# Kernel tuning notes

Hardware: AMD Instinct MI355X
Metric: run time of the kernel (lower is better)

## Reference

```python
import jax, jax.numpy as jnp
import numpy as np

INF = 1.0e6
SIGMA = 1.0
RADIUS = 2.5
M, N, H, K, C_IN, C_OUT = 50000, 50000, 32, 15, 128, 128
EXTENT = 10.0  # spatial extent of the random point cloud


def setup_inputs() -> dict:
    key = jax.random.key(0)
    k1, k2, k3, k4, k5, k6 = jax.random.split(key, 6)
    q_pts = jax.random.uniform(k1, (M, 3), dtype=jnp.float32) * EXTENT
    s_pts = jax.random.uniform(k2, (N, 3), dtype=jnp.float32) * EXTENT
    s_feats = jax.random.normal(k3, (N, C_IN), dtype=jnp.float32)
    neighb_inds = jax.random.randint(k4, (M, H), 0, N, dtype=jnp.int64)
    # kernel points: random points inside sphere of given radius (stand-in for load_kernels)
    kp = jax.random.normal(k5, (K, 3), dtype=jnp.float32)
    kp = kp / jnp.linalg.norm(kp, axis=1, keepdims=True) * (RADIUS * 0.66)
    kernel_points = kp.at[0].set(0.0)  # fixed center point
    # kaiming-uniform-like init
    bound = 1.0 / np.sqrt(C_IN)
    weights = jax.random.uniform(k6, (K, C_IN, C_OUT), dtype=jnp.float32,
                                 minval=-bound, maxval=bound)
    return {"q_pts": q_pts, "s_pts": s_pts, "s_feats": s_feats,
            "neighb_inds": neighb_inds, "kernel_points": kernel_points,
            "weights": weights}


def reference(q_pts, s_pts, s_feats, neighb_inds, kernel_points, weights):
    # pad support points with a far-away point so out-of-range indices get zero influence
    s_pts_pad = jnp.concatenate([s_pts, jnp.full((1, 3), INF, s_pts.dtype)], axis=0)
    neighbors = s_pts_pad[neighb_inds] - q_pts[:, None, :]          # (M, H, 3)
    diffs = neighbors[:, :, None, :] - kernel_points[None, None]    # (M, H, K, 3)
    sq_dist = jnp.sum(diffs * diffs, axis=-1)                       # (M, H, K)
    # linear influence, clipped at 0 (no_grad in torch -> stop_gradient here)
    w = jnp.clip(1.0 - jnp.sqrt(sq_dist) / SIGMA, 0.0)              # (M, H, K)
    neighbor_weights = jax.lax.stop_gradient(jnp.swapaxes(w, 1, 2)) # (M, K, H)
    # gather neighbor features (padded with a zero row)
    feats_pad = jnp.concatenate([s_feats, jnp.zeros((1, s_feats.shape[1]), s_feats.dtype)], axis=0)
    neighbor_feats = feats_pad[neighb_inds]                         # (M, H, C_in)
    weighted_feats = jnp.matmul(neighbor_weights, neighbor_feats)   # (M, K, C_in)
    return jnp.einsum('mkc,kcd->md', weighted_feats, weights)       # (M, C_out)
```

## Files before the change

kernel.cpp:

```cpp
#include <hip/hip_runtime.h>

#define M_Q 50000
#define N_S 50000
#define H_N 32
#define K_P 15
#define C_IN 128
#define C_OUT 128

#define G_QB 64
#define G_NT 256
#define NB_GEO ((M_Q + G_QB - 1) / G_QB)
#define LCAP 64

#define WTF_SLOTS (K_P * 8 * 4 * 64)
#define NB_WCVT (WTF_SLOTS / 256)

#define ENT 96
#define SUBT (ENT / 16)
#define CAPK 12288
#define K2_TILES (CAPK / ENT)

#define WS_WTF_OFF 256
#define WS_WTF_BYTES (WTF_SLOTS * 16)
#define WS_BKT_OFF (WS_WTF_OFF + WS_WTF_BYTES)
#define WS_BKT_BYTES (K_P * CAPK * 8)
#define WS_NEED (WS_BKT_OFF + WS_BKT_BYTES)

typedef __attribute__((ext_vector_type(8))) short s8v;
typedef __attribute__((ext_vector_type(4))) float f4v;
typedef __attribute__((ext_vector_type(4))) float fl4;
typedef __attribute__((ext_vector_type(4))) unsigned u4v;

static __device__ __forceinline__ unsigned f2bf_bits(float x) {
    union { float f; unsigned u; } v; v.f = x;
    return (v.u + 0x7fffu + ((v.u >> 16) & 1u)) >> 16;
}
static __device__ __forceinline__ unsigned pack_bf16(float a, float b) {
    return f2bf_bits(a) | (f2bf_bits(b) << 16);
}

template <typename IT>
__global__ __launch_bounds__(G_NT, 4) void k1_geom(
    const float* __restrict__ q_pts,
    const float* __restrict__ s_pts,
    const IT* __restrict__ inds,
    const float* __restrict__ kp,
    const float* __restrict__ W,
    unsigned* __restrict__ ws_u)
{
    const int b = blockIdx.x;
    const int t = threadIdx.x;

    if (b >= NB_GEO) {
        const int i = (b - NB_GEO) * 256 + t;
        if (i < WTF_SLOTS) {
            const int lane = i & 63;
            const int kk = (i >> 6) & 3;
            const int col = (i >> 8) & 7;
            const int k = i >> 11;
            const int d = col * 16 + (lane & 15);
            const int c0 = kk * 32 + (lane >> 4) * 8;
            unsigned short* dst =
                (unsigned short*)((char*)ws_u + WS_WTF_OFF) + (size_t)i * 8;
            #pragma unroll
            for (int j = 0; j < 8; ++j)
                dst[j] = (unsigned short)f2bf_bits(W[((size_t)k * 128 + c0 + j) * 128 + d]);
        }
        return;
    }

    __shared__ int s_lcnt[K_P];
    __shared__ uint2 s_le[K_P][LCAP];
    __shared__ int s_gb[K_P], s_gc[K_P];

    float kpx[K_P], kpy[K_P], kpz[K_P];
    #pragma unroll
    for (int k = 0; k < K_P; ++k) {
        kpx[k] = kp[k * 3 + 0];
        kpy[k] = kp[k * 3 + 1];
        kpz[k] = kp[k * 3 + 2];
    }

    if (t < K_P) s_lcnt[t] = 0;
    __syncthreads();

    const int qbase = b * G_QB;
    const int lane = t & 63;

    int idxv[8], qgv[8];
    #pragma unroll
    for (int it = 0; it < 8; ++it) {
        const int task = it * G_NT + t;
        const int q = task >> 5, h = task & 31;
        const int qg = qbase + q;
        qgv[it] = qg;
        long long idx = (qg < M_Q) ? (long long)inds[(size_t)qg * H_N + h]
                                   : (long long)N_S;
        idxv[it] = ((unsigned long long)idx < (unsigned long long)N_S) ? (int)idx : -1;
    }
    float px[8], py[8], pz[8], qx[8], qy[8], qz[8];
    #pragma unroll
    for (int it = 0; it < 8; ++it) {
        const int i32 = (idxv[it] >= 0) ? idxv[it] : 0;
        px[it] = s_pts[i32 * 3 + 0];
        py[it] = s_pts[i32 * 3 + 1];
        pz[it] = s_pts[i32 * 3 + 2];
        const int qg = (qgv[it] < M_Q) ? qgv[it] : (M_Q - 1);
        qx[it] = q_pts[qg * 3 + 0];
        qy[it] = q_pts[qg * 3 + 1];
        qz[it] = q_pts[qg * 3 + 2];
    }

    #pragma unroll
    for (int it = 0; it < 8; ++it) {
        const bool valid = (idxv[it] >= 0) & (qgv[it] < M_Q);
        const float rx = valid ? px[it] - qx[it] : 1.0e6f;
        const float ry = valid ? py[it] - qy[it] : 1.0e6f;
        const float rz = valid ? pz[it] - qz[it] : 1.0e6f;
        #pragma unroll
        for (int k = 0; k < K_P; ++k) {
            const float dx = rx - kpx[k];
            const float dy = ry - kpy[k];
            const float dz = rz - kpz[k];
            const float d2 = dx * dx + dy * dy + dz * dz;
            const bool hit = d2 < 1.0f;
            const unsigned long long mask = __ballot(hit);
            if (mask) {
                const int leader = __builtin_ctzll(mask);
                int base = 0;
                if (lane == leader)
                    base = atomicAdd(&s_lcnt[k], (int)__builtin_popcountll(mask));
                base = __shfl(base, leader);
                if (hit) {
                    const int pos = base +
                        (int)__builtin_popcountll(mask & ((1ull << lane) - 1ull));
                    if (pos < LCAP)
                        s_le[k][pos] = make_uint2(
                            ((unsigned)qgv[it] << 16) | (unsigned)idxv[it],
                            __float_as_uint(1.0f - sqrtf(d2)));
                }
            }
        }
    }
    __syncthreads();

    if (t < K_P) {
        const int cl = min(s_lcnt[t], LCAP);
        const int base = (int)atomicAdd(&ws_u[t], (unsigned)cl);
        s_gb[t] = base;
        const int avail = CAPK - base;
        s_gc[t] = max(0, min(cl, avail));
    }
    __syncthreads();

    uint2* bkt = (uint2*)((char*)ws_u + WS_BKT_OFF);
    #pragma unroll
    for (int k = 0; k < K_P; ++k) {
        if (t < s_gc[k])
            bkt[(size_t)k * CAPK + s_gb[k] + t] = s_le[k][t];
    }
}

__global__ __launch_bounds__(256, 3) void k2_gemm(
    const float* __restrict__ s_feats,
    const unsigned* __restrict__ ws_u,
    float* __restrict__ out)
{
    const int k = blockIdx.x;
    const int base = blockIdx.y * ENT;
    const int cnt = min((int)ws_u[k], CAPK);
    int n_e = cnt - base;
    if (n_e <= 0) return;
    if (n_e > ENT) n_e = ENT;

    __shared__ unsigned short s_A[SUBT * 4 * 64 * 8];
    __shared__ unsigned s_mi[ENT];

    const int t = threadIdx.x;
    const int lane = t & 63;
    const int w = t >> 6;
    const int quad = lane >> 4, l15 = lane & 15;

    const unsigned short* Wtf = (const unsigned short*)((const char*)ws_u + WS_WTF_OFF);
    s8v bf[2][4];
    #pragma unroll
    for (int nc = 0; nc < 2; ++nc)
        #pragma unroll
        for (int kk = 0; kk < 4; ++kk)
            bf[nc][kk] = *(const s8v*)(Wtf +
                ((((size_t)k * 8 + (w * 2 + nc)) * 4 + kk) * 64 + lane) * 8);

    const int e = t >> 1, half = t & 1;
    if (e < ENT) {
        const int sub = e >> 4, l15e = e & 15;
        if (e < n_e) {
            const uint2* bkt = (const uint2*)((const char*)ws_u + WS_BKT_OFF)
                               + (size_t)k * CAPK + base;
            const uint2 be = bkt[e];
            const unsigned mi = be.x;
            const float wgt = __uint_as_float(be.y);
            if (half == 0) s_mi[e] = mi;
            const float* fr = s_feats + (size_t)(mi & 0xffffu) * C_IN + half * 64;
            #pragma unroll
            for (int j = 0; j < 4; ++j) {
                const fl4 fa = *(const fl4*)(fr + j * 16);
                const fl4 fb = *(const fl4*)(fr + j * 16 + 4);
                const fl4 fc = *(const fl4*)(fr + j * 16 + 8);
                const fl4 fd = *(const fl4*)(fr + j * 16 + 12);
                u4v g0, g1;
                g0[0] = pack_bf16(wgt * fa.x, wgt * fa.y);
                g0[1] = pack_bf16(wgt * fa.z, wgt * fa.w);
                g0[2] = pack_bf16(wgt * fb.x, wgt * fb.y);
                g0[3] = pack_bf16(wgt * fb.z, wgt * fb.w);
                g1[0] = pack_bf16(wgt * fc.x, wgt * fc.y);
                g1[1] = pack_bf16(wgt * fc.z, wgt * fc.w);
                g1[2] = pack_bf16(wgt * fd.x, wgt * fd.y);
                g1[3] = pack_bf16(wgt * fd.z, wgt * fd.w);
                const int cs = half * 64 + j * 16;
                const int kk = cs >> 5;
                const int qd = (cs >> 3) & 3;
                *(u4v*)&s_A[(size_t)(((sub * 4 + kk) * 64) + qd * 16 + l15e) * 8] = g0;
                *(u4v*)&s_A[(size_t)(((sub * 4 + kk) * 64) + (qd + 1) * 16 + l15e) * 8] = g1;
            }
        } else {
            if (half == 0) s_mi[e] = 0xffffffffu;
            const u4v z = {0u, 0u, 0u, 0u};
            #pragma unroll
            for (int j = 0; j < 4; ++j) {
                const int cs = half * 64 + j * 16;
                const int kk = cs >> 5;
                const int qd = (cs >> 3) & 3;
                *(u4v*)&s_A[(size_t)(((sub * 4 + kk) * 64) + qd * 16 + l15e) * 8] = z;
                *(u4v*)&s_A[(size_t)(((sub * 4 + kk) * 64) + (qd + 1) * 16 + l15e) * 8] = z;
            }
        }
    }
    __syncthreads();

    const f4v zf = {0.0f, 0.0f, 0.0f, 0.0f};
    f4v acc[SUBT][2];
    #pragma unroll
    for (int s = 0; s < SUBT; ++s) { acc[s][0] = zf; acc[s][1] = zf; }

    #pragma unroll
    for (int s = 0; s < SUBT; ++s) {
        s8v af[4];
        #pragma unroll
        for (int kk = 0; kk < 4; ++kk)
            af[kk] = *(const s8v*)&s_A[(size_t)((s * 4 + kk) * 64 + lane) * 8];
        #pragma unroll
        for (int nc = 0; nc < 2; ++nc)
            #pragma unroll
            for (int kk = 0; kk < 4; ++kk)
                acc[s][nc] = __builtin_amdgcn_mfma_f32_16x16x32_bf16(
                    af[kk], bf[nc][kk], acc[s][nc], 0, 0, 0);
    }

    #pragma unroll
    for (int s = 0; s < SUBT; ++s) {
        #pragma unroll
        for (int r = 0; r < 4; ++r) {
            const unsigned mi = s_mi[s * 16 + quad * 4 + r];
            const unsigned m = mi >> 16;
            if (m < M_Q) {
                float* op = out + (size_t)m * C_OUT + w * 32 + l15;
                atomicAdd(op,      acc[s][0][r]);
                atomicAdd(op + 16, acc[s][1][r]);
            }
        }
    }
}

template <typename IT>
__global__ __launch_bounds__(128, 8) void kpconv_v1(
    const float* __restrict__ q_pts, const float* __restrict__ s_pts,
    const float* __restrict__ s_feats, const IT* __restrict__ neighb_inds,
    const float* __restrict__ kernel_points, const float* __restrict__ weights,
    float* __restrict__ out)
{
    __shared__ float s_kp[K_P * 3];
    __shared__ float s_w[K_P][H_N];
    __shared__ int s_idx[H_N];
    __shared__ unsigned s_hmask, s_kmask;
    __shared__ float s_wf[K_P][C_IN];
    const int m = blockIdx.x, tid = threadIdx.x;
    if (tid < K_P * 3) s_kp[tid] = kernel_points[tid];
    if (tid == 0) { s_hmask = 0u; s_kmask = 0u; }
    __syncthreads();
    if (tid < H_N) {
        long long idx = (long long)neighb_inds[(size_t)m * H_N + tid];
        const float qx = q_pts[m * 3], qy = q_pts[m * 3 + 1], qz = q_pts[m * 3 + 2];
        float rx, ry, rz; int idx32;
        if ((unsigned long long)idx < (unsigned long long)N_S) {
            idx32 = (int)idx;
            rx = s_pts[idx32 * 3] - qx; ry = s_pts[idx32 * 3 + 1] - qy; rz = s_pts[idx32 * 3 + 2] - qz;
        } else { idx32 = 0; rx = ry = rz = 1.0e6f; }
        s_idx[tid] = idx32;
        unsigned kmask = 0u;
        #pragma unroll
        for (int k = 0; k < K_P; ++k) {
            const float dx = rx - s_kp[k * 3], dy = ry - s_kp[k * 3 + 1], dz = rz - s_kp[k * 3 + 2];
            const float w = fmaxf(1.0f - sqrtf(dx * dx + dy * dy + dz * dz), 0.0f);
            s_w[k][tid] = w;
            if (w > 0.0f) kmask |= (1u << k);
        }
        if (kmask) { atomicOr(&s_hmask, 1u << tid); atomicOr(&s_kmask, kmask); }
    }
    __syncthreads();
    const unsigned hmask = s_hmask, kmask = s_kmask;
    float wf[K_P];
    #pragma unroll
    for (int k = 0; k < K_P; ++k) wf[k] = 0.0f;
    unsigned hmv = hmask;
    while (hmv) {
        const int h = __builtin_ctz(hmv); hmv &= hmv - 1;
        const float f = s_feats[(size_t)s_idx[h] * C_IN + tid];
        #pragma unroll
        for (int k = 0; k < K_P; ++k) wf[k] = fmaf(s_w[k][h], f, wf[k]);
    }
    #pragma unroll
    for (int k = 0; k < K_P; ++k) s_wf[k][tid] = wf[k];
    __syncthreads();
    float a = 0.0f;
    unsigned km = kmask;
    while (km) {
        const int k = __builtin_ctz(km); km &= km - 1;
        const float* Wk = weights + (size_t)k * C_IN * C_OUT + tid;
        #pragma unroll 8
        for (int c = 0; c < C_IN; ++c) a = fmaf(s_wf[k][c], Wk[(size_t)c * C_OUT], a);
    }
    out[(size_t)m * C_OUT + tid] = a;
}

extern "C" void kernel_launch(void* const* d_in, const int* in_sizes, int n_in,
                              void* d_out, int out_size, void* d_ws, size_t ws_size,
                              hipStream_t stream) {
    const float* q_pts         = (const float*)d_in[0];
    const float* s_pts         = (const float*)d_in[1];
    const float* s_feats       = (const float*)d_in[2];
    const float* kernel_points = (const float*)d_in[4];
    const float* weights       = (const float*)d_in[5];
    float* out = (float*)d_out;
    const bool i64 = (in_sizes[3] == 2 * M_Q * H_N);

    if (ws_size < (size_t)WS_NEED) {
        dim3 grid(M_Q), block(128);
        if (i64)
            kpconv_v1<long long><<<grid, block, 0, stream>>>(
                q_pts, s_pts, s_feats, (const long long*)d_in[3], kernel_points, weights, out);
        else
            kpconv_v1<int><<<grid, block, 0, stream>>>(
                q_pts, s_pts, s_feats, (const int*)d_in[3], kernel_points, weights, out);
        return;
    }

    unsigned* ws_u = (unsigned*)d_ws;
    hipMemsetAsync(d_ws, 0, 64, stream);
    hipMemsetAsync(d_out, 0, (size_t)out_size * sizeof(float), stream);

    dim3 g1(NB_GEO + NB_WCVT), b1(G_NT);
    if (i64)
        k1_geom<long long><<<g1, b1, 0, stream>>>(
            q_pts, s_pts, (const long long*)d_in[3], kernel_points, weights, ws_u);
    else
        k1_geom<int><<<g1, b1, 0, stream>>>(
            q_pts, s_pts, (const int*)d_in[3], kernel_points, weights, ws_u);

    dim3 g2(K_P, K2_TILES), b2(256);
    k2_gemm<<<g2, b2, 0, stream>>>(s_feats, ws_u, out);
}
```

Baseline: 160.5 us.

## Replace scattered float atomics with scratch writes plus per-query gather reduction

The GEMM kernel stops doing atomicAdd scatter into the output for bucketed entries. Instead it writes each entry's 128-wide partial result to a scratch buffer, while the geometry kernel records, for each query, a list of scratch positions. A new reduce kernel sums those rows per query, and an overflow kernel handles lists that exceed capacity. The aim is to remove global float-atomic contention and traffic, at the cost of a large scratch workspace, extra memsets and two more kernel launches.

```diff
diff --git a/kernel.cpp b/kernel.cpp
--- a/kernel.cpp
+++ b/kernel.cpp
@@ -19,12 +19,18 @@
 #define SUBT (ENT / 16)
 #define CAPK 12288
 #define K2_TILES (CAPK / ENT)
-
-#define WS_WTF_OFF 256
-#define WS_WTF_BYTES (WTF_SLOTS * 16)
-#define WS_BKT_OFF (WS_WTF_OFF + WS_WTF_BYTES)
-#define WS_BKT_BYTES (K_P * CAPK * 8)
-#define WS_NEED (WS_BKT_OFF + WS_BKT_BYTES)
+#define SCAP 8192
+#define MLCAP 16
+#define OVFCAP 4096
+
+#define WS_WTF_OFF 128
+#define WS_BKT_OFF 491648
+#define WS_MLC_OFF 1966336
+#define WS_ML_OFF  2166784
+#define WS_OVF_OFF 5366784
+#define WS_SCR_OFF 5399552
+#define WS_NEED_SMALL 1966208
+#define WS_NEED_FULL  68314112ULL
 
 typedef __attribute__((ext_vector_type(8))) short s8v;
 typedef __attribute__((ext_vector_type(4))) float f4v;
@@ -46,7 +52,8 @@
     const IT* __restrict__ inds,
     const float* __restrict__ kp,
     const float* __restrict__ W,
-    unsigned* __restrict__ ws_u)
+    unsigned* __restrict__ ws_u,
+    const int do_full)
 {
     const int b = blockIdx.x;
     const int t = threadIdx.x;
@@ -154,17 +161,34 @@
     __syncthreads();
 
     uint2* bkt = (uint2*)((char*)ws_u + WS_BKT_OFF);
+    unsigned* ml_cnt = ws_u + (WS_MLC_OFF >> 2);
+    unsigned* ml = ws_u + (WS_ML_OFF >> 2);
+    uint2* ovf = (uint2*)((char*)ws_u + WS_OVF_OFF);
     #pragma unroll
     for (int k = 0; k < K_P; ++k) {
-        if (t < s_gc[k])
-            bkt[(size_t)k * CAPK + s_gb[k] + t] = s_le[k][t];
+        if (t < s_gc[k]) {
+            const uint2 ent = s_le[k][t];
+            const int pos = s_gb[k] + t;
+            bkt[(size_t)k * CAPK + pos] = ent;
+            if (do_full && pos < SCAP) {
+                const unsigned m = ent.x >> 16;
+                const unsigned gpos = (unsigned)(k * SCAP + pos);
+                const unsigned j = atomicAdd(&ml_cnt[m], 1u);
+                if (j < MLCAP) ml[(size_t)m * MLCAP + j] = gpos;
+                else {
+                    const unsigned o = atomicAdd(&ws_u[15], 1u);
+                    if (o < OVFCAP) ovf[o] = make_uint2(m, gpos);
+                }
+            }
+        }
     }
 }
 
 __global__ __launch_bounds__(256, 3) void k2_gemm(
     const float* __restrict__ s_feats,
-    const unsigned* __restrict__ ws_u,
-    float* __restrict__ out)
+    unsigned* __restrict__ ws_u,
+    float* __restrict__ out,
+    const int do_full)
 {
     const int k = blockIdx.x;
     const int base = blockIdx.y * ENT;
@@ -180,6 +204,8 @@
     const int lane = t & 63;
     const int w = t >> 6;
     const int quad = lane >> 4, l15 = lane & 15;
+
+    if (do_full && t == 0 && base + n_e > SCAP) atomicAdd(&ws_u[16], 1u);
 
     const unsigned short* Wtf = (const unsigned short*)((const char*)ws_u + WS_WTF_OFF);
     s8v bf[2][4];
@@ -256,19 +282,77 @@
                     af[kk], bf[nc][kk], acc[s][nc], 0, 0, 0);
     }
 
+    float* scratch = (float*)((char*)ws_u + WS_SCR_OFF);
     #pragma unroll
     for (int s = 0; s < SUBT; ++s) {
         #pragma unroll
         for (int r = 0; r < 4; ++r) {
-            const unsigned mi = s_mi[s * 16 + quad * 4 + r];
-            const unsigned m = mi >> 16;
-            if (m < M_Q) {
-                float* op = out + (size_t)m * C_OUT + w * 32 + l15;
-                atomicAdd(op,      acc[s][0][r]);
-                atomicAdd(op + 16, acc[s][1][r]);
+            const int er = s * 16 + quad * 4 + r;
+            if (er < n_e) {
+                const int pos = base + er;
+                if (do_full && pos < SCAP) {
+                    float* sp = scratch + ((size_t)k * SCAP + pos) * 128 + w * 32 + l15;
+                    sp[0]  = acc[s][0][r];
+                    sp[16] = acc[s][1][r];
+                } else {
+                    const unsigned m = s_mi[er] >> 16;
+                    float* op = out + (size_t)m * C_OUT + w * 32 + l15;
+                    atomicAdd(op,      acc[s][0][r]);
+                    atomicAdd(op + 16, acc[s][1][r]);
+                }
             }
         }
     }
+}
+
+__global__ __launch_bounds__(128) void k4_ovf(
+    const unsigned* __restrict__ ws_u, float* __restrict__ out)
+{
+    const float* scratch = (const float*)((const char*)ws_u + WS_SCR_OFF);
+    const uint2* ovf = (const uint2*)((const char*)ws_u + WS_OVF_OFF);
+    unsigned n = ws_u[15];
+    if (n > OVFCAP) n = OVFCAP;
+    for (unsigned i = blockIdx.x; i < n; i += gridDim.x) {
+        const uint2 e = ovf[i];
+        atomicAdd(out + (size_t)e.x * C_OUT + threadIdx.x,
+                  scratch[(size_t)e.y * 128 + threadIdx.x]);
+    }
+}
+
+__global__ __launch_bounds__(256, 4) void k3_reduce(
+    const unsigned* __restrict__ ws_u, float* __restrict__ out)
+{
+    const float* scratch = (const float*)((const char*)ws_u + WS_SCR_OFF);
+    const unsigned* ml_cnt = ws_u + (WS_MLC_OFF >> 2);
+    const unsigned* ml = ws_u + (WS_ML_OFF >> 2);
+
+    const int t = threadIdx.x;
+    const int m = blockIdx.x * 64 + (t >> 2);
+    const int sub = t & 3;
+    if (m >= M_Q) return;
+
+    const bool rd = (ws_u[15] != 0u) || (ws_u[16] != 0u);
+    int cnt = (int)ml_cnt[m];
+    if (cnt > MLCAP) cnt = MLCAP;
+
+    float* op = out + (size_t)m * C_OUT + sub * 32;
+    fl4 a[8];
+    if (rd) {
+        #pragma unroll
+        for (int i = 0; i < 8; ++i) a[i] = ((const fl4*)op)[i];
+    } else {
+        const fl4 z = {0.0f, 0.0f, 0.0f, 0.0f};
+        #pragma unroll
+        for (int i = 0; i < 8; ++i) a[i] = z;
+    }
+    for (int j = 0; j < cnt; ++j) {
+        const unsigned gpos = ml[(size_t)m * MLCAP + j];
+        const fl4* sp = (const fl4*)(scratch + (size_t)gpos * 128 + sub * 32);
+        #pragma unroll
+        for (int i = 0; i < 8; ++i) a[i] += sp[i];
+    }
+    #pragma unroll
+    for (int i = 0; i < 8; ++i) ((fl4*)op)[i] = a[i];
 }
 
 template <typename IT>
@@ -343,7 +427,7 @@
     float* out = (float*)d_out;
     const bool i64 = (in_sizes[3] == 2 * M_Q * H_N);
 
-    if (ws_size < (size_t)WS_NEED) {
+    if (ws_size < (size_t)WS_NEED_SMALL) {
         dim3 grid(M_Q), block(128);
         if (i64)
             kpconv_v1<long long><<<grid, block, 0, stream>>>(
@@ -355,17 +439,26 @@
     }
 
     unsigned* ws_u = (unsigned*)d_ws;
-    hipMemsetAsync(d_ws, 0, 64, stream);
+    const int full = (ws_size >= (size_t)WS_NEED_FULL) ? 1 : 0;
+
+    hipMemsetAsync(d_ws, 0, 128, stream);
+    if (full)
+        hipMemsetAsync((char*)d_ws + WS_MLC_OFF, 0, 200064, stream);
     hipMemsetAsync(d_out, 0, (size_t)out_size * sizeof(float), stream);
 
     dim3 g1(NB_GEO + NB_WCVT), b1(G_NT);
     if (i64)
         k1_geom<long long><<<g1, b1, 0, stream>>>(
-            q_pts, s_pts, (const long long*)d_in[3], kernel_points, weights, ws_u);
+            q_pts, s_pts, (const long long*)d_in[3], kernel_points, weights, ws_u, full);
     else
         k1_geom<int><<<g1, b1, 0, stream>>>(
-            q_pts, s_pts, (const int*)d_in[3], kernel_points, weights, ws_u);
+            q_pts, s_pts, (const int*)d_in[3], kernel_points, weights, ws_u, full);
 
     dim3 g2(K_P, K2_TILES), b2(256);
-    k2_gemm<<<g2, b2, 0, stream>>>(s_feats, ws_u, out);
-}
+    k2_gemm<<<g2, b2, 0, stream>>>(s_feats, ws_u, out, full);
+
+    if (full) {
+        k4_ovf<<<16, 128, 0, stream>>>(ws_u, out);
+        k3_reduce<<<(M_Q + 63) / 64, 256, 0, stream>>>(ws_u, out);
+    }
+}
```

After: 171.0 us. 1.06x slower.
